# Performance work log

Measured on AMD Instinct MI355X. Metric: run time of the kernel, lower is better.

The kernel has to match this reference:

```python
import jax, jax.numpy as jnp
import numpy as np

LN_EPS = 1e-5


def _ln(x, g, b):
    m = jnp.mean(x, axis=-1, keepdims=True)
    v = jnp.mean((x - m) ** 2, axis=-1, keepdims=True)
    return (x - m) / jnp.sqrt(v + LN_EPS) * g + b


def setup_inputs() -> dict:
    key = jax.random.key(0)
    ks = jax.random.split(key, 8)
    B, N, S, D, T = 16, 64, 2048, 1024, 768

    def xavier(k, shape):
        fan_in, fan_out = shape
        lim = (6.0 / (fan_in + fan_out)) ** 0.5
        return jax.random.uniform(k, shape, minval=-lim, maxval=lim, dtype=jnp.float32)

    return {
        "prev_states": jax.random.normal(ks[0], (B, N, D), dtype=jnp.float32),
        "input_tokens": jax.random.normal(ks[1], (B, S, T), dtype=jnp.float32),
        # input_projection (token_dim -> state_dim)
        "W_proj": xavier(ks[2], (T, D)),
        "b_proj": jnp.zeros((D,), jnp.float32),
        # three LayerNorms
        "g_state": jnp.ones((D,), jnp.float32), "beta_state": jnp.zeros((D,), jnp.float32),
        "g_input": jnp.ones((D,), jnp.float32), "beta_input": jnp.zeros((D,), jnp.float32),
        "g_out": jnp.ones((D,), jnp.float32), "beta_out": jnp.zeros((D,), jnp.float32),
        # GRU gates (2D -> D); update-gate bias initialized to -1 as in the module
        "W_u": xavier(ks[3], (2 * D, D)), "b_u": jnp.full((D,), -1.0, jnp.float32),
        "W_r": xavier(ks[4], (2 * D, D)), "b_r": jnp.zeros((D,), jnp.float32),
        "W_n": xavier(ks[5], (2 * D, D)), "b_n": jnp.zeros((D,), jnp.float32),
    }


def reference(prev_states, input_tokens, W_proj, b_proj,
              g_state, beta_state, g_input, beta_input, g_out, beta_out,
              W_u, b_u, W_r, b_r, W_n, b_n):
    D = prev_states.shape[-1]
    # project tokens to state dim: (B,S,D)
    tok = input_tokens @ W_proj + b_proj
    # attention routing (routing_weights=None path)
    scores = jnp.einsum('bnd,bsd->bns', prev_states, tok) / jnp.sqrt(jnp.float32(D))
    attn = jax.nn.softmax(scores, axis=-1)
    routed = jnp.einsum('bns,bsd->bnd', attn, tok)  # (B,N,D)
    # GRU-style gated update, vectorized over the num_states axis
    ps_n = _ln(prev_states, g_state, beta_state)
    in_n = _ln(routed, g_input, beta_input)
    concat = jnp.concatenate([ps_n, in_n], axis=-1)  # (B,N,2D)
    u = jax.nn.sigmoid(concat @ W_u + b_u)
    r = jax.nn.sigmoid(concat @ W_r + b_r)
    reset_in = jnp.concatenate([r * ps_n, in_n], axis=-1)
    cand = jnp.tanh(reset_in @ W_n + b_n)  # dropout is identity in eval
    new_state = (1.0 - u) * prev_states + u * cand
    return _ln(new_state, g_out, beta_out)
```

## Files before the change

### kernel.cpp

```cpp
#include <hip/hip_runtime.h>
#include <stdint.h>

typedef __attribute__((ext_vector_type(4))) float floatx4;
typedef __attribute__((ext_vector_type(8))) short shortx8;

#define LN_EPS 1e-5f

__device__ __forceinline__ unsigned short f2b(float f) {
  unsigned u = __builtin_bit_cast(unsigned, f);
  u = (u + 0x7FFFu + ((u >> 16) & 1u)) >> 16;
  return (unsigned short)u;
}
__device__ __forceinline__ float b2f(unsigned short h) {
  return __builtin_bit_cast(float, (unsigned)h << 16);
}

__device__ __forceinline__ void g2l16(const unsigned short* g, unsigned short* l) {
  __builtin_amdgcn_global_load_lds(
      (const __attribute__((address_space(1))) unsigned int*)g,
      (__attribute__((address_space(3))) unsigned int*)l, 16, 0, 0);
}

__device__ __forceinline__ float wave_sum(float v) {
#pragma unroll
  for (int o = 32; o; o >>= 1) v += __shfl_down(v, o, 64);
  return v;
}
__device__ __forceinline__ float block_sum(float v, float* s) {
  v = wave_sum(v);
  __syncthreads();
  if ((threadIdx.x & 63) == 0) s[threadIdx.x >> 6] = v;
  __syncthreads();
  return s[0] + s[1] + s[2] + s[3];
}

__global__ __launch_bounds__(256) void k_prep(
    const float* __restrict__ prev, unsigned short* __restrict__ psb,
    const float* __restrict__ toks, unsigned short* __restrict__ tokb,
    const float* __restrict__ wp, unsigned short* __restrict__ wpb,
    const float* __restrict__ Wu, const float* __restrict__ Wr,
    const float* __restrict__ Wn,
    unsigned short* __restrict__ Wtur, unsigned short* __restrict__ Wtn,
    unsigned short* __restrict__ Wtp, float* __restrict__ rs) {
  __shared__ float tile[32][33];
  const int bid = blockIdx.x;
  if (bid < 26368) {
    if (bid == 0) {
      floatx4 z = {0.f, 0.f, 0.f, 0.f};
      *(floatx4*)(rs + threadIdx.x * 4) = z;
    }
    const long chunk = (long)bid * 256 + threadIdx.x;
    const float* src;
    unsigned short* dst;
    long i;
    if (chunk < 262144) { src = prev; dst = psb; i = chunk * 4; }
    else if (chunk < 6553600) { src = toks; dst = tokb; i = (chunk - 262144) * 4; }
    else { src = wp; dst = wpb; i = (chunk - 6553600) * 4; }
    floatx4 v = *(const floatx4*)(src + i);
    unsigned short t4[4];
#pragma unroll
    for (int j = 0; j < 4; j++) t4[j] = f2b(v[j]);
    *(uint2*)(dst + i) = *(uint2*)t4;
    return;
  }
  int t = bid - 26368;
  const float* in;
  unsigned short* out;
  int K, kx, ny;
  if (t < 6144) {
    const int which = t >> 11;
    const int t2 = t & 2047;
    kx = t2 & 63;
    ny = t2 >> 6;
    K = 2048;
    in = which == 0 ? Wu : (which == 1 ? Wr : Wn);
    out = which == 0 ? Wtur : (which == 1 ? Wtur + 1024 * 2048 : Wtn);
  } else {
    const int t2 = t - 6144;
    kx = t2 % 24;
    ny = t2 / 24;
    K = 768;
    in = wp;
    out = Wtp;
  }
  const int N = 1024;
  const int k0 = kx * 32, n0 = ny * 32;
  const int tx = threadIdx.x & 31, ty = threadIdx.x >> 5;
#pragma unroll
  for (int i = 0; i < 32; i += 8)
    tile[ty + i][tx] = in[(long)(k0 + ty + i) * N + n0 + tx];
  __syncthreads();
#pragma unroll
  for (int i = 0; i < 32; i += 8)
    out[(long)(n0 + ty + i) * K + k0 + tx] = f2b(tile[tx][ty + i]);
}

__global__ __launch_bounds__(256) void k_gemm64(
    const unsigned short* __restrict__ A, int lda,
    const unsigned short* __restrict__ Bt, int ldb,
    int K,
    const float* __restrict__ bias, const float* __restrict__ bias2,
    int mode,
    void* __restrict__ out, int ldc,
    unsigned short* __restrict__ out2,
    const unsigned short* __restrict__ aux_psn,
    const float* __restrict__ aux_u, const float* __restrict__ aux_prev) {
  __shared__ unsigned short As[2][64 * 64];
  __shared__ unsigned short Bs[2][64 * 64];
  const int tid = threadIdx.x;
  const int wave = tid >> 6, lane = tid & 63;
  const int flat = blockIdx.x + blockIdx.y * gridDim.x;
  const int q = (gridDim.x * gridDim.y) >> 3;
  const int swz = (flat & 7) * q + (flat >> 3);
  const int m0 = (swz % gridDim.x) * 64;
  const int n0 = (swz / gridDim.x) * 64;
  const int wm = wave & 1, wn = wave >> 1;
  const int l16 = lane & 15, quad = lane >> 4;
  const int srow8 = lane >> 3;
  const int c8 = ((lane & 7) ^ srow8) * 8;

  const unsigned short* gA[2];
  const unsigned short* gB[2];
  int lOff[2];
#pragma unroll
  for (int j = 0; j < 2; j++) {
    const int rb = wave * 16 + j * 8;
    gA[j] = A + (long)(m0 + rb + srow8) * lda + c8;
    gB[j] = Bt + (long)(n0 + rb + srow8) * ldb + c8;
    lOff[j] = rb * 64;
  }
  int offA[2][2], offB[2][2];
#pragma unroll
  for (int ks = 0; ks < 2; ks++)
#pragma unroll
    for (int i = 0; i < 2; i++) {
      int r = wm * 32 + i * 16 + l16;
      offA[ks][i] = r * 64 + (((ks * 4 + quad) ^ (r & 7)) * 8);
      r = wn * 32 + i * 16 + l16;
      offB[ks][i] = r * 64 + (((ks * 4 + quad) ^ (r & 7)) * 8);
    }

  floatx4 acc[2][2] = {};

#pragma unroll
  for (int j = 0; j < 2; j++) {
    g2l16(gA[j], &As[0][lOff[j]]);
    g2l16(gB[j], &Bs[0][lOff[j]]);
  }
  __syncthreads();

  const int nt = K >> 6;
  for (int t = 0; t < nt; t++) {
    const int cur = t & 1;
    if (t + 1 < nt) {
      const int kn = (t + 1) << 6;
#pragma unroll
      for (int j = 0; j < 2; j++) {
        g2l16(gA[j] + kn, &As[cur ^ 1][lOff[j]]);
        g2l16(gB[j] + kn, &Bs[cur ^ 1][lOff[j]]);
      }
    }
#pragma unroll
    for (int ks = 0; ks < 2; ks++) {
      shortx8 af[2], bf[2];
#pragma unroll
      for (int i = 0; i < 2; i++) af[i] = *(const shortx8*)&As[cur][offA[ks][i]];
#pragma unroll
      for (int j = 0; j < 2; j++) bf[j] = *(const shortx8*)&Bs[cur][offB[ks][j]];
#pragma unroll
      for (int i = 0; i < 2; i++)
#pragma unroll
        for (int j = 0; j < 2; j++)
          acc[i][j] = __builtin_amdgcn_mfma_f32_16x16x32_bf16(af[i], bf[j], acc[i][j], 0, 0, 0);
    }
    __syncthreads();
  }

#pragma unroll
  for (int i = 0; i < 2; i++)
#pragma unroll
    for (int j = 0; j < 2; j++) {
      const int rbase = m0 + wm * 32 + i * 16 + quad * 4;
      const int c = n0 + wn * 32 + j * 16 + l16;
      float bval = 0.0f;
      if (bias) bval = (mode == 5 && c >= 1024) ? bias2[c - 1024] : bias[c];
#pragma unroll
      for (int r = 0; r < 4; r++) {
        const int row = rbase + r;
        float v = acc[i][j][r] + bval;
        if (mode == 1) {
          out2[(long)row * ldc + c] = f2b(v);
        } else if (mode == 3) {
          float cand = tanhf(v);
          float u = aux_u[(long)row * 1024 + c];
          float p = aux_prev[(long)row * 1024 + c];
          ((float*)out)[(long)row * ldc + c] = (1.0f - u) * p + u * cand;
        } else if (mode == 6) {
          ((float*)out)[(long)row * ldc + c] = v + aux_u[row] * bias2[c];
        } else {
          if (c < 1024) {
            ((float*)out)[(long)row * 1024 + c] = 1.0f / (1.0f + expf(-v));
          } else {
            const int cc = c - 1024;
            float rr = 1.0f / (1.0f + expf(-v));
            out2[(long)row * 2048 + cc] = f2b(rr * b2f(aux_psn[(long)row * 2048 + cc]));
          }
        }
      }
    }
}

__global__ __launch_bounds__(256) void k_scores(
    const unsigned short* __restrict__ A, long sAb, int lda,
    const unsigned short* __restrict__ Bt, long sBb, int ldb,
    int K, float scale,
    unsigned short* __restrict__ out2, int ldc, long sCb,
    float* __restrict__ rs) {
  __shared__ unsigned short As[2][64 * 64];
  __shared__ unsigned short Bs[2][64 * 64];
  const int tid = threadIdx.x;
  const int wave = tid >> 6, lane = tid & 63;
  const int b = blockIdx.z;
  const int m0 = blockIdx.x * 64, n0 = blockIdx.y * 64;
  const int wm = wave & 1, wn = wave >> 1;
  const int l16 = lane & 15, quad = lane >> 4;
  const int srow8 = lane >> 3;
  const int c8 = ((lane & 7) ^ srow8) * 8;
  const unsigned short* Ab = A + (long)b * sAb;
  const unsigned short* Bb = Bt + (long)b * sBb;

  const unsigned short* gA[2];
  const unsigned short* gB[2];
  int lOff[2];
#pragma unroll
  for (int j = 0; j < 2; j++) {
    const int rb = wave * 16 + j * 8;
    gA[j] = Ab + (long)(m0 + rb + srow8) * lda + c8;
    gB[j] = Bb + (long)(n0 + rb + srow8) * ldb + c8;
    lOff[j] = rb * 64;
  }
  int offA[2][2], offB[2][2];
#pragma unroll
  for (int ks = 0; ks < 2; ks++)
#pragma unroll
    for (int i = 0; i < 2; i++) {
      int r = wm * 32 + i * 16 + l16;
      offA[ks][i] = r * 64 + (((ks * 4 + quad) ^ (r & 7)) * 8);
      r = wn * 32 + i * 16 + l16;
      offB[ks][i] = r * 64 + (((ks * 4 + quad) ^ (r & 7)) * 8);
    }

  floatx4 acc[2][2] = {};

#pragma unroll
  for (int j = 0; j < 2; j++) {
    g2l16(gA[j], &As[0][lOff[j]]);
    g2l16(gB[j], &Bs[0][lOff[j]]);
  }
  __syncthreads();

  const int nt = K >> 6;
  for (int t = 0; t < nt; t++) {
    const int cur = t & 1;
    if (t + 1 < nt) {
      const int kn = (t + 1) << 6;
#pragma unroll
      for (int j = 0; j < 2; j++) {
        g2l16(gA[j] + kn, &As[cur ^ 1][lOff[j]]);
        g2l16(gB[j] + kn, &Bs[cur ^ 1][lOff[j]]);
      }
    }
#pragma unroll
    for (int ks = 0; ks < 2; ks++) {
      shortx8 af[2], bf[2];
#pragma unroll
      for (int i = 0; i < 2; i++) af[i] = *(const shortx8*)&As[cur][offA[ks][i]];
#pragma unroll
      for (int j = 0; j < 2; j++) bf[j] = *(const shortx8*)&Bs[cur][offB[ks][j]];
#pragma unroll
      for (int i = 0; i < 2; i++)
#pragma unroll
        for (int j = 0; j < 2; j++)
          acc[i][j] = __builtin_amdgcn_mfma_f32_16x16x32_bf16(af[i], bf[j], acc[i][j], 0, 0, 0);
    }
    __syncthreads();
  }

#pragma unroll
  for (int i = 0; i < 2; i++) {
    float psum[4] = {0.f, 0.f, 0.f, 0.f};
#pragma unroll
    for (int j = 0; j < 2; j++) {
      const int rbase = m0 + wm * 32 + i * 16 + quad * 4;
      const int c = n0 + wn * 32 + j * 16 + l16;
#pragma unroll
      for (int r = 0; r < 4; r++) {
        const float e = expf(acc[i][j][r] * scale);
        out2[(long)b * sCb + (long)(rbase + r) * ldc + c] = f2b(e);
        psum[r] += e;
      }
    }
#pragma unroll
    for (int r = 0; r < 4; r++) {
      float s = psum[r];
      s += __shfl_xor(s, 1, 64);
      s += __shfl_xor(s, 2, 64);
      s += __shfl_xor(s, 4, 64);
      s += __shfl_xor(s, 8, 64);
      if (l16 == 0)
        atomicAdd(rs + (long)b * 64 + m0 + wm * 32 + i * 16 + quad * 4 + r, s);
    }
  }
}

__global__ __launch_bounds__(256) void k_routed_mfma(
    const unsigned short* __restrict__ attnb,
    const unsigned short* __restrict__ tok,
    unsigned short* __restrict__ rwb) {
  __shared__ unsigned short As[64 * 40];
  __shared__ unsigned short Bs[32 * 66];
  const int nt = blockIdx.x, b = blockIdx.y;
  const int tid = threadIdx.x;
  const int wave = tid >> 6, lane = tid & 63;
  const int wm = wave & 1, wn = wave >> 1;
  const int l16 = lane & 15, quad = lane >> 4;
  const int n0 = nt * 64;
  const long abase = (long)b * 131072;
  const long tbase = (long)b * 1572864;
  const int srow = tid >> 2, skc = (tid & 3) * 8;
  const int bk = tid >> 3, bd = (tid & 7) * 8;

  floatx4 acc[2][2] = {};

  uint4 pa = *(const uint4*)(attnb + abase + (long)srow * 2048 + skc);
  uint4 pb = *(const uint4*)(tok + tbase + (long)bk * 768 + n0 + bd);

  for (int k0 = 0; k0 < 2048; k0 += 32) {
    *(uint4*)&As[srow * 40 + skc] = pa;
    {
      const unsigned* pv = (const unsigned*)&pb;
      unsigned short* dst = &Bs[bk * 66 + bd];
#pragma unroll
      for (int w2 = 0; w2 < 4; w2++) *(unsigned*)(dst + w2 * 2) = pv[w2];
    }
    if (k0 + 32 < 2048) {
      pa = *(const uint4*)(attnb + abase + (long)srow * 2048 + (k0 + 32) + skc);
      pb = *(const uint4*)(tok + tbase + (long)(k0 + 32 + bk) * 768 + n0 + bd);
    }
    asm volatile("s_waitcnt lgkmcnt(0)" ::: "memory");
    __builtin_amdgcn_s_barrier();
    __builtin_amdgcn_sched_barrier(0);

    shortx8 a0 = *(const shortx8*)&As[(wm * 32 + 0  + l16) * 40 + quad * 8];
    shortx8 a1 = *(const shortx8*)&As[(wm * 32 + 16 + l16) * 40 + quad * 8];
    shortx8 b0, b1;
#pragma unroll
    for (int j = 0; j < 8; j++) {
      b0[j] = *(const short*)&Bs[(quad * 8 + j) * 66 + wn * 32 + l16];
      b1[j] = *(const short*)&Bs[(quad * 8 + j) * 66 + wn * 32 + 16 + l16];
    }
    acc[0][0] = __builtin_amdgcn_mfma_f32_16x16x32_bf16(a0, b0, acc[0][0], 0, 0, 0);
    acc[0][1] = __builtin_amdgcn_mfma_f32_16x16x32_bf16(a0, b1, acc[0][1], 0, 0, 0);
    acc[1][0] = __builtin_amdgcn_mfma_f32_16x16x32_bf16(a1, b0, acc[1][0], 0, 0, 0);
    acc[1][1] = __builtin_amdgcn_mfma_f32_16x16x32_bf16(a1, b1, acc[1][1], 0, 0, 0);
    __builtin_amdgcn_s_barrier();
  }

#pragma unroll
  for (int im = 0; im < 2; im++)
#pragma unroll
    for (int in_ = 0; in_ < 2; in_++) {
      const int rbase = wm * 32 + im * 16 + quad * 4;
      const int c = n0 + wn * 32 + in_ * 16 + l16;
#pragma unroll
      for (int r = 0; r < 4; r++)
        rwb[((long)b * 64 + rbase + r) * 768 + c] = f2b(acc[im][in_][r]);
    }
}

__global__ __launch_bounds__(256) void k_ln2(
    const float* __restrict__ prev, const float* __restrict__ routed,
    const float* __restrict__ g_st, const float* __restrict__ be_st,
    const float* __restrict__ g_in, const float* __restrict__ be_in,
    unsigned short* __restrict__ conc, unsigned short* __restrict__ candA) {
  __shared__ float scr[4];
  const long r = blockIdx.x & 1023;
  const bool second = blockIdx.x >= 1024;
  const int t = threadIdx.x;
  floatx4 v;
  const float *g, *be;
  if (!second) {
    v = *(const floatx4*)(prev + r * 1024 + t * 4);
    g = g_st; be = be_st;
  } else {
    v = *(const floatx4*)(routed + r * 1024 + t * 4);
    g = g_in; be = be_in;
  }
  float s1 = v[0] + v[1] + v[2] + v[3];
  float s2 = v[0] * v[0] + v[1] * v[1] + v[2] * v[2] + v[3] * v[3];
  s1 = block_sum(s1, scr);
  s2 = block_sum(s2, scr);
  const float mean = s1 * (1.0f / 1024.0f);
  const float var = s2 * (1.0f / 1024.0f) - mean * mean;
  const float rstd = rsqrtf(var + LN_EPS);
#pragma unroll
  for (int i = 0; i < 4; i++) {
    const int d = t * 4 + i;
    const float y = (v[i] - mean) * rstd * g[d] + be[d];
    const unsigned short h = f2b(y);
    if (!second) {
      conc[r * 2048 + d] = h;
    } else {
      conc[r * 2048 + 1024 + d] = h;
      candA[r * 2048 + 1024 + d] = h;
    }
  }
}

__global__ __launch_bounds__(256) void k_ln_out(
    const float* __restrict__ in, const float* __restrict__ g,
    const float* __restrict__ be, float* __restrict__ out) {
  __shared__ float scr[4];
  const long r = blockIdx.x;
  const int t = threadIdx.x;
  floatx4 v = *(const floatx4*)(in + r * 1024 + t * 4);
  float s1 = v[0] + v[1] + v[2] + v[3];
  float s2 = v[0] * v[0] + v[1] * v[1] + v[2] * v[2] + v[3] * v[3];
  s1 = block_sum(s1, scr);
  s2 = block_sum(s2, scr);
  const float mean = s1 * (1.0f / 1024.0f);
  const float var = s2 * (1.0f / 1024.0f) - mean * mean;
  const float rstd = rsqrtf(var + LN_EPS);
  floatx4 o;
#pragma unroll
  for (int i = 0; i < 4; i++) {
    const int d = t * 4 + i;
    o[i] = (v[i] - mean) * rstd * g[d] + be[d];
  }
  *(floatx4*)(out + r * 1024 + t * 4) = o;
}

extern "C" void kernel_launch(void* const* d_in, const int* in_sizes, int n_in,
                              void* d_out, int out_size, void* d_ws, size_t ws_size,
                              hipStream_t stream) {
  (void)in_sizes; (void)n_in; (void)out_size; (void)ws_size;
  const float* prev  = (const float*)d_in[0];
  const float* toks  = (const float*)d_in[1];
  const float* Wp    = (const float*)d_in[2];
  const float* bp    = (const float*)d_in[3];
  const float* g_st  = (const float*)d_in[4];
  const float* be_st = (const float*)d_in[5];
  const float* g_in  = (const float*)d_in[6];
  const float* be_in = (const float*)d_in[7];
  const float* g_o   = (const float*)d_in[8];
  const float* be_o  = (const float*)d_in[9];
  const float* Wu    = (const float*)d_in[10];
  const float* bu    = (const float*)d_in[11];
  const float* Wr    = (const float*)d_in[12];
  const float* br    = (const float*)d_in[13];
  const float* Wn    = (const float*)d_in[14];
  const float* bn    = (const float*)d_in[15];
  float* out = (float*)d_out;

  char* ws = (char*)d_ws;
  unsigned short* tokb  = (unsigned short*)ws; ws += 50331648;
  unsigned short* psb   = (unsigned short*)ws; ws += 2097152;
  unsigned short* Wpb   = (unsigned short*)ws; ws += 1572864;
  unsigned short* Wtp   = (unsigned short*)ws; ws += 1572864;
  unsigned short* pwb   = (unsigned short*)ws; ws += 1572864;
  unsigned short* attnb = (unsigned short*)ws; ws += 4194304;
  float*          rowsum= (float*)ws;          ws += 4096;
  unsigned short* rwb   = (unsigned short*)ws; ws += 1572864;
  float*          routed= (float*)ws;          ws += 4194304;
  unsigned short* conc  = (unsigned short*)ws; ws += 4194304;
  unsigned short* candA = (unsigned short*)ws; ws += 4194304;
  float*          ubuf  = (float*)ws;          ws += 4194304;
  float*          ns    = (float*)ws;          ws += 4194304;
  unsigned short* Wtur  = (unsigned short*)ws; ws += 8388608;
  unsigned short* Wtn   = (unsigned short*)ws; ws += 4194304;

  const dim3 blk(256);

  k_prep<<<dim3(33280), blk, 0, stream>>>(prev, psb, toks, tokb, Wp, Wpb,
                                          Wu, Wr, Wn, Wtur, Wtn, Wtp, rowsum);
  k_gemm64<<<dim3(16, 12), blk, 0, stream>>>(
      psb, 1024, Wpb, 1024, 1024,
      nullptr, nullptr, 1,
      nullptr, 768, pwb, nullptr, nullptr, nullptr);
  k_scores<<<dim3(1, 32, 16), blk, 0, stream>>>(
      pwb, 49152L, 768, tokb, 1572864L, 768, 768, 0.03125f,
      attnb, 2048, 131072L, rowsum);
  k_routed_mfma<<<dim3(12, 16), blk, 0, stream>>>(attnb, tokb, rwb);
  k_gemm64<<<dim3(16, 16), blk, 0, stream>>>(
      rwb, 768, Wtp, 768, 768,
      nullptr, bp, 6,
      (void*)routed, 1024, nullptr, nullptr, rowsum, nullptr);
  k_ln2<<<dim3(2048), blk, 0, stream>>>(prev, routed, g_st, be_st, g_in, be_in,
                                        conc, candA);
  k_gemm64<<<dim3(16, 32), blk, 0, stream>>>(
      conc, 2048, Wtur, 2048, 2048,
      bu, br, 5,
      (void*)ubuf, 1024, candA, conc, nullptr, nullptr);
  k_gemm64<<<dim3(16, 16), blk, 0, stream>>>(
      candA, 2048, Wtn, 2048, 2048,
      bn, nullptr, 3,
      (void*)ns, 1024, nullptr, nullptr, ubuf, prev);
  k_ln_out<<<dim3(1024), blk, 0, stream>>>(ns, g_o, be_o, out);
}
```

Before: 337.3 us.

## Fuse fp32-to-bf16 token conversion into score and routing kernels, split-K routed GEMM

Drops the separate pass that converted the 48 MB token tensor to bf16. The scores and routed kernels now read fp32 tokens directly and convert them while staging into LDS, which saves one full write plus re-read of the bf16 copy. The routed GEMM is split into two K chunks to double its block count, with a small kernel that sums the partials and converts them to bf16. The cost is that tokens are read as fp32 twice, at double the bytes per read. It also adds an extra launch and a partial-sum buffer.

```diff
diff --git a/kernel.cpp b/kernel.cpp
--- a/kernel.cpp
+++ b/kernel.cpp
@@ -36,7 +36,6 @@
 
 __global__ __launch_bounds__(256) void k_prep(
     const float* __restrict__ prev, unsigned short* __restrict__ psb,
-    const float* __restrict__ toks, unsigned short* __restrict__ tokb,
     const float* __restrict__ wp, unsigned short* __restrict__ wpb,
     const float* __restrict__ Wu, const float* __restrict__ Wr,
     const float* __restrict__ Wn,
@@ -44,26 +43,25 @@
     unsigned short* __restrict__ Wtp, float* __restrict__ rs) {
   __shared__ float tile[32][33];
   const int bid = blockIdx.x;
-  if (bid < 26368) {
+  if (bid < 896) {
     if (bid == 0) {
       floatx4 z = {0.f, 0.f, 0.f, 0.f};
       *(floatx4*)(rs + threadIdx.x * 4) = z;
     }
-    const long chunk = (long)bid * 256 + threadIdx.x;
     const float* src;
     unsigned short* dst;
     long i;
-    if (chunk < 262144) { src = prev; dst = psb; i = chunk * 4; }
-    else if (chunk < 6553600) { src = toks; dst = tokb; i = (chunk - 262144) * 4; }
-    else { src = wp; dst = wpb; i = (chunk - 6553600) * 4; }
-    floatx4 v = *(const floatx4*)(src + i);
-    unsigned short t4[4];
-#pragma unroll
-    for (int j = 0; j < 4; j++) t4[j] = f2b(v[j]);
-    *(uint2*)(dst + i) = *(uint2*)t4;
+    if (bid < 512) { src = prev; dst = psb; i = ((long)bid * 256 + threadIdx.x) * 8; }
+    else { src = wp; dst = wpb; i = ((long)(bid - 512) * 256 + threadIdx.x) * 8; }
+    floatx4 v0 = *(const floatx4*)(src + i);
+    floatx4 v1 = *(const floatx4*)(src + i + 4);
+    unsigned short t8[8];
+#pragma unroll
+    for (int j = 0; j < 4; j++) { t8[j] = f2b(v0[j]); t8[4 + j] = f2b(v1[j]); }
+    *(uint4*)(dst + i) = *(uint4*)t8;
     return;
   }
-  int t = bid - 26368;
+  int t = bid - 896;
   const float* in;
   unsigned short* out;
   int K, kx, ny;
@@ -212,7 +210,7 @@
 
 __global__ __launch_bounds__(256) void k_scores(
     const unsigned short* __restrict__ A, long sAb, int lda,
-    const unsigned short* __restrict__ Bt, long sBb, int ldb,
+    const float* __restrict__ toksf,
     int K, float scale,
     unsigned short* __restrict__ out2, int ldc, long sCb,
     float* __restrict__ rs) {
@@ -221,22 +219,21 @@
   const int tid = threadIdx.x;
   const int wave = tid >> 6, lane = tid & 63;
   const int b = blockIdx.z;
-  const int m0 = blockIdx.x * 64, n0 = blockIdx.y * 64;
+  const int m0 = 0, n0 = blockIdx.y * 64;
   const int wm = wave & 1, wn = wave >> 1;
   const int l16 = lane & 15, quad = lane >> 4;
   const int srow8 = lane >> 3;
   const int c8 = ((lane & 7) ^ srow8) * 8;
   const unsigned short* Ab = A + (long)b * sAb;
-  const unsigned short* Bb = Bt + (long)b * sBb;
 
   const unsigned short* gA[2];
-  const unsigned short* gB[2];
+  const float* gBf[2];
   int lOff[2];
 #pragma unroll
   for (int j = 0; j < 2; j++) {
     const int rb = wave * 16 + j * 8;
     gA[j] = Ab + (long)(m0 + rb + srow8) * lda + c8;
-    gB[j] = Bb + (long)(n0 + rb + srow8) * ldb + c8;
+    gBf[j] = toksf + (long)b * 1572864 + (long)(n0 + rb + srow8) * 768 + c8;
     lOff[j] = rb * 64;
   }
   int offA[2][2], offB[2][2];
@@ -255,19 +252,26 @@
 #pragma unroll
   for (int j = 0; j < 2; j++) {
     g2l16(gA[j], &As[0][lOff[j]]);
-    g2l16(gB[j], &Bs[0][lOff[j]]);
+    floatx4 v0 = *(const floatx4*)(gBf[j]);
+    floatx4 v1 = *(const floatx4*)(gBf[j] + 4);
+    unsigned short t8[8];
+#pragma unroll
+    for (int i = 0; i < 4; i++) { t8[i] = f2b(v0[i]); t8[4 + i] = f2b(v1[i]); }
+    *(uint4*)&Bs[0][lOff[j] + lane * 8] = *(uint4*)t8;
   }
   __syncthreads();
 
   const int nt = K >> 6;
   for (int t = 0; t < nt; t++) {
     const int cur = t & 1;
+    floatx4 w0[2], w1[2];
     if (t + 1 < nt) {
       const int kn = (t + 1) << 6;
 #pragma unroll
       for (int j = 0; j < 2; j++) {
         g2l16(gA[j] + kn, &As[cur ^ 1][lOff[j]]);
-        g2l16(gB[j] + kn, &Bs[cur ^ 1][lOff[j]]);
+        w0[j] = *(const floatx4*)(gBf[j] + kn);
+        w1[j] = *(const floatx4*)(gBf[j] + kn + 4);
       }
     }
 #pragma unroll
@@ -282,6 +286,15 @@
 #pragma unroll
         for (int j = 0; j < 2; j++)
           acc[i][j] = __builtin_amdgcn_mfma_f32_16x16x32_bf16(af[i], bf[j], acc[i][j], 0, 0, 0);
+    }
+    if (t + 1 < nt) {
+#pragma unroll
+      for (int j = 0; j < 2; j++) {
+        unsigned short t8[8];
+#pragma unroll
+        for (int i = 0; i < 4; i++) { t8[i] = f2b(w0[j][i]); t8[4 + i] = f2b(w1[j][i]); }
+        *(uint4*)&Bs[cur ^ 1][lOff[j] + lane * 8] = *(uint4*)t8;
+      }
     }
     __syncthreads();
   }
@@ -315,37 +328,41 @@
 
 __global__ __launch_bounds__(256) void k_routed_mfma(
     const unsigned short* __restrict__ attnb,
-    const unsigned short* __restrict__ tok,
-    unsigned short* __restrict__ rwb) {
+    const float* __restrict__ tokf,
+    float* __restrict__ parts) {
   __shared__ unsigned short As[64 * 40];
   __shared__ unsigned short Bs[32 * 66];
-  const int nt = blockIdx.x, b = blockIdx.y;
+  const int kc = blockIdx.x, nt = blockIdx.y, b = blockIdx.z;
   const int tid = threadIdx.x;
   const int wave = tid >> 6, lane = tid & 63;
   const int wm = wave & 1, wn = wave >> 1;
   const int l16 = lane & 15, quad = lane >> 4;
   const int n0 = nt * 64;
-  const long abase = (long)b * 131072;
-  const long tbase = (long)b * 1572864;
+  const long abase = (long)b * 131072 + (long)kc * 1024;
+  const long tbase = ((long)b * 2048 + (long)kc * 1024) * 768;
   const int srow = tid >> 2, skc = (tid & 3) * 8;
   const int bk = tid >> 3, bd = (tid & 7) * 8;
 
   floatx4 acc[2][2] = {};
 
   uint4 pa = *(const uint4*)(attnb + abase + (long)srow * 2048 + skc);
-  uint4 pb = *(const uint4*)(tok + tbase + (long)bk * 768 + n0 + bd);
-
-  for (int k0 = 0; k0 < 2048; k0 += 32) {
+  floatx4 f0 = *(const floatx4*)(tokf + tbase + (long)bk * 768 + n0 + bd);
+  floatx4 f1 = *(const floatx4*)(tokf + tbase + (long)bk * 768 + n0 + bd + 4);
+
+  for (int k0 = 0; k0 < 1024; k0 += 32) {
     *(uint4*)&As[srow * 40 + skc] = pa;
     {
-      const unsigned* pv = (const unsigned*)&pb;
+      unsigned short t8[8];
+#pragma unroll
+      for (int i = 0; i < 4; i++) { t8[i] = f2b(f0[i]); t8[4 + i] = f2b(f1[i]); }
       unsigned short* dst = &Bs[bk * 66 + bd];
 #pragma unroll
-      for (int w2 = 0; w2 < 4; w2++) *(unsigned*)(dst + w2 * 2) = pv[w2];
-    }
-    if (k0 + 32 < 2048) {
+      for (int w2 = 0; w2 < 4; w2++) *(unsigned*)(dst + w2 * 2) = ((unsigned*)t8)[w2];
+    }
+    if (k0 + 32 < 1024) {
       pa = *(const uint4*)(attnb + abase + (long)srow * 2048 + (k0 + 32) + skc);
-      pb = *(const uint4*)(tok + tbase + (long)(k0 + 32 + bk) * 768 + n0 + bd);
+      f0 = *(const floatx4*)(tokf + tbase + (long)(k0 + 32 + bk) * 768 + n0 + bd);
+      f1 = *(const floatx4*)(tokf + tbase + (long)(k0 + 32 + bk) * 768 + n0 + bd + 4);
     }
     asm volatile("s_waitcnt lgkmcnt(0)" ::: "memory");
     __builtin_amdgcn_s_barrier();
@@ -374,8 +391,20 @@
       const int c = n0 + wn * 32 + in_ * 16 + l16;
 #pragma unroll
       for (int r = 0; r < 4; r++)
-        rwb[((long)b * 64 + rbase + r) * 768 + c] = f2b(acc[im][in_][r]);
-    }
+        parts[(long)kc * 786432 + ((long)b * 64 + rbase + r) * 768 + c] =
+            acc[im][in_][r];
+    }
+}
+
+__global__ __launch_bounds__(256) void k_sumcvt(
+    const float* __restrict__ parts, unsigned short* __restrict__ out) {
+  const long i = ((long)blockIdx.x * 256 + threadIdx.x) * 4;
+  floatx4 v = *(const floatx4*)(parts + i);
+  floatx4 w = *(const floatx4*)(parts + 786432 + i);
+  unsigned short t4[4];
+#pragma unroll
+  for (int j = 0; j < 4; j++) t4[j] = f2b(v[j] + w[j]);
+  *(uint2*)(out + i) = *(uint2*)t4;
 }
 
 __global__ __launch_bounds__(256) void k_ln2(
@@ -463,13 +492,13 @@
   float* out = (float*)d_out;
 
   char* ws = (char*)d_ws;
-  unsigned short* tokb  = (unsigned short*)ws; ws += 50331648;
   unsigned short* psb   = (unsigned short*)ws; ws += 2097152;
   unsigned short* Wpb   = (unsigned short*)ws; ws += 1572864;
   unsigned short* Wtp   = (unsigned short*)ws; ws += 1572864;
   unsigned short* pwb   = (unsigned short*)ws; ws += 1572864;
   unsigned short* attnb = (unsigned short*)ws; ws += 4194304;
   float*          rowsum= (float*)ws;          ws += 4096;
+  float*          parts = (float*)ws;          ws += 6291456;
   unsigned short* rwb   = (unsigned short*)ws; ws += 1572864;
   float*          routed= (float*)ws;          ws += 4194304;
   unsigned short* conc  = (unsigned short*)ws; ws += 4194304;
@@ -481,16 +510,17 @@
 
   const dim3 blk(256);
 
-  k_prep<<<dim3(33280), blk, 0, stream>>>(prev, psb, toks, tokb, Wp, Wpb,
-                                          Wu, Wr, Wn, Wtur, Wtn, Wtp, rowsum);
+  k_prep<<<dim3(7808), blk, 0, stream>>>(prev, psb, Wp, Wpb,
+                                         Wu, Wr, Wn, Wtur, Wtn, Wtp, rowsum);
   k_gemm64<<<dim3(16, 12), blk, 0, stream>>>(
       psb, 1024, Wpb, 1024, 1024,
       nullptr, nullptr, 1,
       nullptr, 768, pwb, nullptr, nullptr, nullptr);
   k_scores<<<dim3(1, 32, 16), blk, 0, stream>>>(
-      pwb, 49152L, 768, tokb, 1572864L, 768, 768, 0.03125f,
+      pwb, 49152L, 768, toks, 768, 0.03125f,
       attnb, 2048, 131072L, rowsum);
-  k_routed_mfma<<<dim3(12, 16), blk, 0, stream>>>(attnb, tokb, rwb);
+  k_routed_mfma<<<dim3(2, 12, 16), blk, 0, stream>>>(attnb, toks, parts);
+  k_sumcvt<<<dim3(768), blk, 0, stream>>>(parts, rwb);
   k_gemm64<<<dim3(16, 16), blk, 0, stream>>>(
       rwb, 768, Wtp, 768, 768,
       nullptr, bp, 6,
```

After: 322.2 us. 1.05x faster.
